# Optimization experiments

Measured on AMD Instinct MI355X. Metric: run time of the kernel, lower is better.

The kernel has to match this reference:

```python
import jax, jax.numpy as jnp
import numpy as np
import math

NEG = -10000.0  # original uses -10000.0, not -inf

def setup_inputs() -> dict:
    key = jax.random.key(0)
    B, S, H, D = 2, 2048, 16, 128
    qkv = jax.random.normal(key, (B, S, 3, H, D), dtype=jnp.float32)
    return {"qkv": qkv}

def reference(qkv):
    # qkv: (B, S, 3, H, D); causal softmax attention, dropout p=0 (identity)
    B, S, _, H, D = qkv.shape
    q = qkv[:, :, 0]  # (B,S,H,D)
    k = qkv[:, :, 1]
    v = qkv[:, :, 2]
    softmax_scale = 1.0 / math.sqrt(D)
    # scores: (B, H, T, S)
    scores = jnp.einsum('bthd,bshd->bhts', q, k * softmax_scale)
    causal_mask = jnp.triu(jnp.full((S, S), NEG, dtype=scores.dtype), 1)
    scores = scores + causal_mask  # broadcast over (B,H)
    attention = jax.nn.softmax(scores, axis=-1)
    out = jnp.einsum('bhts,bshd->bthd', attention, v)  # (B,T,H,D)
    return out
```

## Files before the change

kernel.cpp:

```cpp
#include <hip/hip_runtime.h>
#include <hip/hip_bf16.h>
#include <math.h>

typedef __bf16 bf16;
typedef bf16 bf16x8 __attribute__((ext_vector_type(8)));
typedef float floatx4 __attribute__((ext_vector_type(4)));

#define MFMA16(a, b, c) __builtin_amdgcn_mfma_f32_16x16x32_bf16(a, b, c, 0, 0, 0)

constexpr int Bb = 2, Ss = 2048, Hh = 16, Dd = 128;
constexpr float SCALE = 0.08838834764831845f;

__constant__ int U_QT[40] = {0,1,2,3, 4,4, 5,5, 6,6, 7,7, 8,8,8, 9,9,9, 10,10,10,
                             11,11,11, 12,12,12,12, 13,13,13,13, 14,14,14,14, 15,15,15,15};
__constant__ int U_S[40]  = {0,0,0,0, 0,10, 0,12, 0,14, 0,16, 0,12,24, 0,14,27, 0,15,30,
                             0,16,32, 0,13,26,39, 0,14,28,42, 0,15,30,45, 0,16,32,48};
__constant__ int U_E[40]  = {4,8,12,16, 10,20, 12,24, 14,28, 16,32, 12,24,36, 14,27,40,
                             15,30,44, 16,32,48, 13,26,39,52, 14,28,42,56, 15,30,45,60,
                             16,32,48,64};
__constant__ int RS0[12] = {0,2,4,6,8,11,14,17,20,24,28,32};
__constant__ int RN[12]  = {2,2,2,2,3,3,3,3,4,4,4,4};

__global__ __launch_bounds__(256) void prep_pack(const float* __restrict__ qkv,
                                                 bf16* __restrict__ QP,
                                                 bf16* __restrict__ KP,
                                                 bf16* __restrict__ VP) {
  __shared__ bf16 Vt[64 * 136];

  const int tid = threadIdx.x;
  const int w = tid >> 6, lane = tid & 63, quad = lane >> 4, l15 = lane & 15;
  const int qt = blockIdx.x, bh = blockIdx.y;
  const int b = bh >> 4, h = bh & 15;
  const int q0 = qt * 64;
  const size_t rs = (size_t)3 * Hh * Dd;
  const float* base = qkv + (size_t)b * Ss * rs + (size_t)h * Dd;

  for (int idx = tid; idx < 64 * 32; idx += 256) {
    const int row = idx >> 5;
    const int c4 = (idx & 31) << 2;
    const float* p = base + (size_t)(q0 + row) * rs + 2 * Hh * Dd + c4;
    float4 x = *(const float4*)p;
    bf16* d = Vt + row * 136 + c4;
    d[0] = (bf16)x.x; d[1] = (bf16)x.y; d[2] = (bf16)x.z; d[3] = (bf16)x.w;
  }

  {
    bf16* blob = QP + (size_t)(bh * 32 + qt) * 8192;
    const float* src = base + (size_t)(q0 + 4 * l15 + w) * rs;
    for (int kk = 0; kk < 4; ++kk) {
      const float* s8 = src + kk * 32 + quad * 8;
      float4 x0 = *(const float4*)s8, x1 = *(const float4*)(s8 + 4);
      bf16x8 f;
      f[0] = (bf16)(x0.x * SCALE); f[1] = (bf16)(x0.y * SCALE);
      f[2] = (bf16)(x0.z * SCALE); f[3] = (bf16)(x0.w * SCALE);
      f[4] = (bf16)(x1.x * SCALE); f[5] = (bf16)(x1.y * SCALE);
      f[6] = (bf16)(x1.z * SCALE); f[7] = (bf16)(x1.w * SCALE);
      *(bf16x8*)(blob + (size_t)(((w * 4 + kk) * 4 + quad) * 16 + l15) * 8) = f;
    }
  }

  const int ktg = qt * 2 + (w >> 1);
  {
    const int c = w & 1;
    bf16* blob = KP + (size_t)(bh * 64 + ktg) * 4096;
    const float* src = base + (size_t)(ktg * 32 + c * 16 + l15) * rs + Hh * Dd;
    for (int kk = 0; kk < 4; ++kk) {
      const float* s8 = src + kk * 32 + quad * 8;
      float4 x0 = *(const float4*)s8, x1 = *(const float4*)(s8 + 4);
      bf16x8 f;
      f[0] = (bf16)x0.x; f[1] = (bf16)x0.y; f[2] = (bf16)x0.z; f[3] = (bf16)x0.w;
      f[4] = (bf16)x1.x; f[5] = (bf16)x1.y; f[6] = (bf16)x1.z; f[7] = (bf16)x1.w;
      *(bf16x8*)(blob + (size_t)(((c * 4 + kk) * 4 + quad) * 16 + l15) * 8) = f;
    }
  }

  __syncthreads();

  {
    bf16* blob = VP + (size_t)(bh * 64 + ktg) * 4096;
    const int kloc = (w >> 1) * 32;
    for (int ti = 0; ti < 4; ++ti) {
      const int t = (w & 1) * 4 + ti;
      const int d = t * 16 + l15;
      bf16x8 f;
      for (int j = 0; j < 8; ++j) f[j] = Vt[(kloc + quad * 8 + j) * 136 + d];
      *(bf16x8*)(blob + (size_t)((t * 4 + quad) * 16 + l15) * 8) = f;
    }
  }
}

__device__ __forceinline__ void cp1k(const bf16* src, bf16* dst, int lane) {
  __builtin_amdgcn_global_load_lds(
      (__attribute__((address_space(1))) void*)(src + lane * 8),
      (__attribute__((address_space(3))) void*)dst, 16, 0, 0);
}

__global__ __launch_bounds__(256, 3) void attn_fwd_s(const bf16* __restrict__ QP,
                                                     const bf16* __restrict__ KP,
                                                     const bf16* __restrict__ VP,
                                                     float* __restrict__ out,
                                                     bf16* __restrict__ PO,
                                                     float* __restrict__ PL) {
  __shared__ bf16 Kl[2][4096];
  __shared__ bf16 Vl[2][4096];
  __shared__ bf16 Pl[4 * 32 * 40];

  const int tid = threadIdx.x;
  const int w = tid >> 6, lane = tid & 63, quad = lane >> 4, l15 = lane & 15;
  const int u = blockIdx.x;
  const int bh = blockIdx.y;
  const int b = bh >> 4, h = bh & 15;
  const int qt = U_QT[u];
  const int ks = U_S[u], ke = U_E[u];
  const int q0 = qt * 128;

  bf16x8 qf[2][4];
  for (int m = 0; m < 2; ++m) {
    const bf16* qp = QP + (size_t)(bh * 32 + 2 * qt + m) * 8192;
    for (int kk = 0; kk < 4; ++kk)
      qf[m][kk] = *(const bf16x8*)(qp + (size_t)(((w * 4 + kk) * 4 + quad) * 16 + l15) * 8);
  }

  floatx4 acc_o[2][8];
  for (int m = 0; m < 2; ++m)
    for (int t = 0; t < 8; ++t) acc_o[m][t] = (floatx4){0.f, 0.f, 0.f, 0.f};
  float l_part[2][4] = {{0.f, 0.f, 0.f, 0.f}, {0.f, 0.f, 0.f, 0.f}};

  const size_t bh64 = (size_t)bh * 64;
  bf16* pw = &Pl[w * 1280];

  auto stage = [&](int kt, int nb) {
    const bf16* kblob = KP + (bh64 + kt) * 4096;
    const bf16* vblob = VP + (bh64 + kt) * 4096;
    if (w < 2) {
      for (int i = 0; i < 4; ++i) {
        const int g = w * 4 + i;
        cp1k(kblob + g * 512, &Kl[nb][g * 512], lane);
      }
    } else {
      for (int i = 0; i < 4; ++i) {
        const int g = (w - 2) * 4 + i;
        cp1k(vblob + g * 512, &Vl[nb][g * 512], lane);
      }
    }
  };

  stage(ks, 0);
  __syncthreads();

  for (int it = 0, kt = ks; kt < ke; ++kt, ++it) {
    const int nb = it & 1;
    if (kt + 1 < ke) stage(kt + 1, nb ^ 1);

    const bool do0 = (kt <= 4 * qt + 1);
    const bool mask0 = (kt >= 4 * qt);
    const bool mask1 = (kt >= 4 * qt + 2);
    const int kbase = kt * 32;

    floatx4 s0[2], s1[2];
    s0[0] = s0[1] = s1[0] = s1[1] = (floatx4){0.f, 0.f, 0.f, 0.f};
    for (int c = 0; c < 2; ++c)
      for (int kk = 0; kk < 4; ++kk) {
        bf16x8 bfrag = *(const bf16x8*)(&Kl[nb][((c * 4 + kk) * 64 + lane) * 8]);
        if (do0) s0[c] = MFMA16(qf[0][kk], bfrag, s0[c]);
        s1[c] = MFMA16(qf[1][kk], bfrag, s1[c]);
      }

    if (do0) {
      float p[2][4];
      if (mask0) {
        for (int c = 0; c < 2; ++c) {
          const int colg = kbase + c * 16 + l15;
          for (int r = 0; r < 4; ++r) {
            const int rowg = q0 + 4 * (quad * 4 + r) + w;
            p[c][r] = __expf((colg > rowg) ? -10000.f : s0[c][r]);
          }
        }
      } else {
        for (int c = 0; c < 2; ++c)
          for (int r = 0; r < 4; ++r) p[c][r] = __expf(s0[c][r]);
      }
      for (int r = 0; r < 4; ++r) l_part[0][r] += p[0][r] + p[1][r];
      for (int c = 0; c < 2; ++c)
        for (int r = 0; r < 4; ++r)
          pw[(quad * 4 + r) * 40 + c * 16 + l15] = (bf16)p[c][r];
    }
    {
      float p[2][4];
      if (mask1) {
        for (int c = 0; c < 2; ++c) {
          const int colg = kbase + c * 16 + l15;
          for (int r = 0; r < 4; ++r) {
            const int rowg = q0 + 64 + 4 * (quad * 4 + r) + w;
            p[c][r] = __expf((colg > rowg) ? -10000.f : s1[c][r]);
          }
        }
      } else {
        for (int c = 0; c < 2; ++c)
          for (int r = 0; r < 4; ++r) p[c][r] = __expf(s1[c][r]);
      }
      for (int r = 0; r < 4; ++r) l_part[1][r] += p[0][r] + p[1][r];
      for (int c = 0; c < 2; ++c)
        for (int r = 0; r < 4; ++r)
          pw[(16 + quad * 4 + r) * 40 + c * 16 + l15] = (bf16)p[c][r];
    }

    bf16x8 af0, af1;
    if (do0) af0 = *(const bf16x8*)(&Pl[w * 1280 + l15 * 40 + quad * 8]);
    af1 = *(const bf16x8*)(&Pl[w * 1280 + (16 + l15) * 40 + quad * 8]);
    for (int t = 0; t < 8; ++t) {
      bf16x8 vfrag = *(const bf16x8*)(&Vl[nb][(t * 64 + lane) * 8]);
      if (do0) acc_o[0][t] = MFMA16(af0, vfrag, acc_o[0][t]);
      acc_o[1][t] = MFMA16(af1, vfrag, acc_o[1][t]);
    }

    __syncthreads();
  }

  if (u < 4) {
    for (int m = 0; m < 2; ++m) {
      float rl[4];
      for (int r = 0; r < 4; ++r) {
        float l = l_part[m][r];
        for (int off = 1; off < 16; off <<= 1) l += __shfl_xor(l, off);
        rl[r] = 1.0f / l;
      }
      for (int r = 0; r < 4; ++r) {
        const int rowg = q0 + m * 64 + 4 * (quad * 4 + r) + w;
        float* op = out + ((size_t)(b * Ss + rowg) * Hh + h) * Dd + l15;
        for (int t = 0; t < 8; ++t) op[t * 16] = acc_o[m][t][r] * rl[r];
      }
    }
  } else {
    const int slot = bh * 36 + (u - 4);
    bf16* po = PO + (size_t)slot * 16384;
    float* pl = PL + (size_t)slot * 128;
    for (int m = 0; m < 2; ++m) {
      for (int r = 0; r < 4; ++r) {
        float l = l_part[m][r];
        for (int off = 1; off < 16; off <<= 1) l += __shfl_xor(l, off);
        if (l15 == 0) pl[m * 64 + 4 * (quad * 4 + r) + w] = l;
      }
      for (int r = 0; r < 4; ++r) {
        const int rloc = m * 64 + 4 * (quad * 4 + r) + w;
        bf16* pp = po + rloc * 128 + l15;
        for (int t = 0; t < 8; ++t) pp[t * 16] = (bf16)acc_o[m][t][r];
      }
    }
  }
}

__global__ __launch_bounds__(256) void reduce_merge(const bf16* __restrict__ PO,
                                                    const float* __restrict__ PL,
                                                    float* __restrict__ out) {
  const int qt = 4 + blockIdx.x;
  const int bh = blockIdx.y;
  const int b = bh >> 4, h = bh & 15;
  const int s0 = bh * 36 + RS0[blockIdx.x];
  const int nch = RN[blockIdx.x];
  const int tid = threadIdx.x;

  __shared__ float linv[128];
  if (tid < 128) {
    float l = 0.f;
    for (int c = 0; c < nch; ++c) l += PL[(size_t)(s0 + c) * 128 + tid];
    linv[tid] = 1.0f / l;
  }
  __syncthreads();

  const int q0 = qt * 128;
  for (int t = 0; t < 32; ++t) {
    const int idx2 = t * 256 + tid;
    const int row = idx2 >> 6;
    const int d = (idx2 & 63) * 2;
    float v0 = 0.f, v1 = 0.f;
    for (int c = 0; c < nch; ++c) {
      const bf16* p = PO + (size_t)(s0 + c) * 16384 + row * 128 + d;
      v0 += (float)p[0];
      v1 += (float)p[1];
    }
    float* op = out + ((size_t)(b * Ss + q0 + row) * Hh + h) * Dd + d;
    const float rl = linv[row];
    op[0] = v0 * rl;
    op[1] = v1 * rl;
  }
}

__global__ __launch_bounds__(256, 3) void attn_fwd_mono(const bf16* __restrict__ QP,
                                                        const bf16* __restrict__ KP,
                                                        const bf16* __restrict__ VP,
                                                        float* __restrict__ out) {
  __shared__ bf16 Kl[2][4096];
  __shared__ bf16 Vl[2][4096];
  __shared__ bf16 Pl[4 * 32 * 40];

  const int tid = threadIdx.x;
  const int w = tid >> 6, lane = tid & 63, quad = lane >> 4, l15 = lane & 15;
  const int qt = (gridDim.x - 1) - blockIdx.x;
  const int bh = blockIdx.y;
  const int b = bh >> 4, h = bh & 15;
  const int q0 = qt * 128;

  bf16x8 qf[2][4];
  for (int m = 0; m < 2; ++m) {
    const bf16* qp = QP + (size_t)(bh * 32 + 2 * qt + m) * 8192;
    for (int kk = 0; kk < 4; ++kk)
      qf[m][kk] = *(const bf16x8*)(qp + (size_t)(((w * 4 + kk) * 4 + quad) * 16 + l15) * 8);
  }

  floatx4 acc_o[2][8];
  for (int m = 0; m < 2; ++m)
    for (int t = 0; t < 8; ++t) acc_o[m][t] = (floatx4){0.f, 0.f, 0.f, 0.f};
  float l_part[2][4] = {{0.f, 0.f, 0.f, 0.f}, {0.f, 0.f, 0.f, 0.f}};

  const int ntiles = 4 * qt + 4;
  const size_t bh64 = (size_t)bh * 64;
  bf16* pw = &Pl[w * 1280];

  auto stage = [&](int kt, int nb) {
    const bf16* kblob = KP + (bh64 + kt) * 4096;
    const bf16* vblob = VP + (bh64 + kt) * 4096;
    if (w < 2) {
      for (int i = 0; i < 4; ++i) {
        const int g = w * 4 + i;
        cp1k(kblob + g * 512, &Kl[nb][g * 512], lane);
      }
    } else {
      for (int i = 0; i < 4; ++i) {
        const int g = (w - 2) * 4 + i;
        cp1k(vblob + g * 512, &Vl[nb][g * 512], lane);
      }
    }
  };

  stage(0, 0);
  __syncthreads();

  for (int kt = 0; kt < ntiles; ++kt) {
    const int nb = kt & 1;
    if (kt + 1 < ntiles) stage(kt + 1, nb ^ 1);

    const bool do0 = (kt <= 4 * qt + 1);
    const bool mask0 = (kt >= 4 * qt);
    const bool mask1 = (kt >= 4 * qt + 2);
    const int kbase = kt * 32;

    floatx4 s0[2], s1[2];
    s0[0] = s0[1] = s1[0] = s1[1] = (floatx4){0.f, 0.f, 0.f, 0.f};
    for (int c = 0; c < 2; ++c)
      for (int kk = 0; kk < 4; ++kk) {
        bf16x8 bfrag = *(const bf16x8*)(&Kl[nb][((c * 4 + kk) * 64 + lane) * 8]);
        if (do0) s0[c] = MFMA16(qf[0][kk], bfrag, s0[c]);
        s1[c] = MFMA16(qf[1][kk], bfrag, s1[c]);
      }

    if (do0) {
      float p[2][4];
      if (mask0) {
        for (int c = 0; c < 2; ++c) {
          const int colg = kbase + c * 16 + l15;
          for (int r = 0; r < 4; ++r) {
            const int rowg = q0 + 4 * (quad * 4 + r) + w;
            p[c][r] = __expf((colg > rowg) ? -10000.f : s0[c][r]);
          }
        }
      } else {
        for (int c = 0; c < 2; ++c)
          for (int r = 0; r < 4; ++r) p[c][r] = __expf(s0[c][r]);
      }
      for (int r = 0; r < 4; ++r) l_part[0][r] += p[0][r] + p[1][r];
      for (int c = 0; c < 2; ++c)
        for (int r = 0; r < 4; ++r)
          pw[(quad * 4 + r) * 40 + c * 16 + l15] = (bf16)p[c][r];
    }
    {
      float p[2][4];
      if (mask1) {
        for (int c = 0; c < 2; ++c) {
          const int colg = kbase + c * 16 + l15;
          for (int r = 0; r < 4; ++r) {
            const int rowg = q0 + 64 + 4 * (quad * 4 + r) + w;
            p[c][r] = __expf((colg > rowg) ? -10000.f : s1[c][r]);
          }
        }
      } else {
        for (int c = 0; c < 2; ++c)
          for (int r = 0; r < 4; ++r) p[c][r] = __expf(s1[c][r]);
      }
      for (int r = 0; r < 4; ++r) l_part[1][r] += p[0][r] + p[1][r];
      for (int c = 0; c < 2; ++c)
        for (int r = 0; r < 4; ++r)
          pw[(16 + quad * 4 + r) * 40 + c * 16 + l15] = (bf16)p[c][r];
    }

    bf16x8 af0, af1;
    if (do0) af0 = *(const bf16x8*)(&Pl[w * 1280 + l15 * 40 + quad * 8]);
    af1 = *(const bf16x8*)(&Pl[w * 1280 + (16 + l15) * 40 + quad * 8]);
    for (int t = 0; t < 8; ++t) {
      bf16x8 vfrag = *(const bf16x8*)(&Vl[nb][(t * 64 + lane) * 8]);
      if (do0) acc_o[0][t] = MFMA16(af0, vfrag, acc_o[0][t]);
      acc_o[1][t] = MFMA16(af1, vfrag, acc_o[1][t]);
    }

    __syncthreads();
  }

  for (int m = 0; m < 2; ++m) {
    float rl[4];
    for (int r = 0; r < 4; ++r) {
      float l = l_part[m][r];
      for (int off = 1; off < 16; off <<= 1) l += __shfl_xor(l, off);
      rl[r] = 1.0f / l;
    }
    for (int r = 0; r < 4; ++r) {
      const int rowg = q0 + m * 64 + 4 * (quad * 4 + r) + w;
      float* op = out + ((size_t)(b * Ss + rowg) * Hh + h) * Dd + l15;
      for (int t = 0; t < 8; ++t) op[t * 16] = acc_o[m][t][r] * rl[r];
    }
  }
}

extern "C" void kernel_launch(void* const* d_in, const int* in_sizes, int n_in,
                              void* d_out, int out_size, void* d_ws, size_t ws_size,
                              hipStream_t stream) {
  const float* qkv = (const float*)d_in[0];
  float* out = (float*)d_out;
  char* ws = (char*)d_ws;
  bf16* QP = (bf16*)ws;
  bf16* KP = (bf16*)(ws + (size_t)16 * 1024 * 1024);
  bf16* VP = (bf16*)(ws + (size_t)32 * 1024 * 1024);
  bf16* PO = (bf16*)(ws + (size_t)48 * 1024 * 1024);
  float* PL = (float*)(ws + (size_t)48 * 1024 * 1024 + (size_t)1152 * 32768);

  const size_t need = (size_t)48 * 1024 * 1024 + (size_t)1152 * 32768 + (size_t)1152 * 512;

  prep_pack<<<dim3(32, 32), 256, 0, stream>>>(qkv, QP, KP, VP);
  if (ws_size >= need) {
    attn_fwd_s<<<dim3(40, 32), 256, 0, stream>>>(QP, KP, VP, out, PO, PL);
    reduce_merge<<<dim3(12, 32), 256, 0, stream>>>(PO, PL, out);
  } else {
    attn_fwd_mono<<<dim3(16, 32), 256, 0, stream>>>(QP, KP, VP, out);
  }
}
```

Before: 259.8 us.

## Flatten grids bh-fastest, stage partial stores through LDS, vectorize merge kernel

Grids move from 2D to 1D with the batch-head index varying fastest. This changes block dispatch order so that blocks sharing a query tile run together, which should improve L2 locality and balance heavy causal tiles across CUs. The split-K partial outputs are now staged through shared memory and written with 16-byte coalesced stores instead of scattered 2-byte stores. The merge kernel now uses 512 threads, each reading 16-byte bf16 vectors and writing float4 outputs. The cost is extra syncthreads in the epilogue and higher register use in the reduce kernel.

After: 231.0 us. 1.12x faster.

```diff
diff --git a/kernel.cpp b/kernel.cpp
--- a/kernel.cpp
+++ b/kernel.cpp
@@ -29,7 +29,7 @@
 
   const int tid = threadIdx.x;
   const int w = tid >> 6, lane = tid & 63, quad = lane >> 4, l15 = lane & 15;
-  const int qt = blockIdx.x, bh = blockIdx.y;
+  const int bh = blockIdx.x & 31, qt = blockIdx.x >> 5;
   const int b = bh >> 4, h = bh & 15;
   const int q0 = qt * 64;
   const size_t rs = (size_t)3 * Hh * Dd;
@@ -107,8 +107,8 @@
 
   const int tid = threadIdx.x;
   const int w = tid >> 6, lane = tid & 63, quad = lane >> 4, l15 = lane & 15;
-  const int u = blockIdx.x;
-  const int bh = blockIdx.y;
+  const int bh = blockIdx.x & 31;
+  const int u = blockIdx.x >> 5;
   const int b = bh >> 4, h = bh & 15;
   const int qt = U_QT[u];
   const int ks = U_S[u], ke = U_E[u];
@@ -235,54 +235,67 @@
     const int slot = bh * 36 + (u - 4);
     bf16* po = PO + (size_t)slot * 16384;
     float* pl = PL + (size_t)slot * 128;
+    bf16* Ol = &Kl[0][0];
     for (int m = 0; m < 2; ++m) {
       for (int r = 0; r < 4; ++r) {
         float l = l_part[m][r];
         for (int off = 1; off < 16; off <<= 1) l += __shfl_xor(l, off);
         if (l15 == 0) pl[m * 64 + 4 * (quad * 4 + r) + w] = l;
       }
+      __syncthreads();
       for (int r = 0; r < 4; ++r) {
-        const int rloc = m * 64 + 4 * (quad * 4 + r) + w;
-        bf16* pp = po + rloc * 128 + l15;
-        for (int t = 0; t < 8; ++t) pp[t * 16] = (bf16)acc_o[m][t][r];
-      }
-    }
-  }
-}
-
-__global__ __launch_bounds__(256) void reduce_merge(const bf16* __restrict__ PO,
+        const int rl = 4 * (quad * 4 + r) + w;
+        bf16* op = Ol + rl * 128 + l15;
+        for (int t = 0; t < 8; ++t) op[t * 16] = (bf16)acc_o[m][t][r];
+      }
+      __syncthreads();
+      for (int k = 0; k < 4; ++k) {
+        bf16x8 v = *(const bf16x8*)(Ol + k * 2048 + tid * 8);
+        *(bf16x8*)(po + m * 8192 + k * 2048 + tid * 8) = v;
+      }
+    }
+  }
+}
+
+__global__ __launch_bounds__(512) void reduce_merge(const bf16* __restrict__ PO,
                                                     const float* __restrict__ PL,
                                                     float* __restrict__ out) {
-  const int qt = 4 + blockIdx.x;
-  const int bh = blockIdx.y;
+  const int bh = blockIdx.x & 31;
+  const int j = blockIdx.x >> 5;
   const int b = bh >> 4, h = bh & 15;
-  const int s0 = bh * 36 + RS0[blockIdx.x];
-  const int nch = RN[blockIdx.x];
+  const int s0 = bh * 36 + RS0[j];
+  const int nch = RN[j];
   const int tid = threadIdx.x;
-
-  __shared__ float linv[128];
-  if (tid < 128) {
-    float l = 0.f;
-    for (int c = 0; c < nch; ++c) l += PL[(size_t)(s0 + c) * 128 + tid];
-    linv[tid] = 1.0f / l;
-  }
-  __syncthreads();
-
-  const int q0 = qt * 128;
-  for (int t = 0; t < 32; ++t) {
-    const int idx2 = t * 256 + tid;
-    const int row = idx2 >> 6;
-    const int d = (idx2 & 63) * 2;
-    float v0 = 0.f, v1 = 0.f;
-    for (int c = 0; c < nch; ++c) {
-      const bf16* p = PO + (size_t)(s0 + c) * 16384 + row * 128 + d;
-      v0 += (float)p[0];
-      v1 += (float)p[1];
-    }
-    float* op = out + ((size_t)(b * Ss + q0 + row) * Hh + h) * Dd + d;
-    const float rl = linv[row];
-    op[0] = v0 * rl;
-    op[1] = v1 * rl;
+  const int row = tid >> 2;
+  const int d0 = (tid & 3) << 5;
+
+  float l = 0.f;
+  for (int c = 0; c < nch; ++c) l += PL[(size_t)(s0 + c) * 128 + row];
+  const float rl = 1.0f / l;
+
+  float acc[32];
+#pragma unroll
+  for (int e = 0; e < 32; ++e) acc[e] = 0.f;
+  for (int c = 0; c < nch; ++c) {
+    const bf16* p = PO + (size_t)(s0 + c) * 16384 + row * 128 + d0;
+#pragma unroll
+    for (int k = 0; k < 4; ++k) {
+      bf16x8 v = *(const bf16x8*)(p + k * 8);
+#pragma unroll
+      for (int e = 0; e < 8; ++e) acc[k * 8 + e] += (float)v[e];
+    }
+  }
+
+  const int q0 = (4 + j) * 128;
+  float* op = out + ((size_t)(b * Ss + q0 + row) * Hh + h) * Dd + d0;
+#pragma unroll
+  for (int k = 0; k < 8; ++k) {
+    float4 o;
+    o.x = acc[k * 4 + 0] * rl;
+    o.y = acc[k * 4 + 1] * rl;
+    o.z = acc[k * 4 + 2] * rl;
+    o.w = acc[k * 4 + 3] * rl;
+    *(float4*)(op + k * 4) = o;
   }
 }
 
@@ -434,10 +447,10 @@
 
   const size_t need = (size_t)48 * 1024 * 1024 + (size_t)1152 * 32768 + (size_t)1152 * 512;
 
-  prep_pack<<<dim3(32, 32), 256, 0, stream>>>(qkv, QP, KP, VP);
+  prep_pack<<<dim3(1024), 256, 0, stream>>>(qkv, QP, KP, VP);
   if (ws_size >= need) {
-    attn_fwd_s<<<dim3(40, 32), 256, 0, stream>>>(QP, KP, VP, out, PO, PL);
-    reduce_merge<<<dim3(12, 32), 256, 0, stream>>>(PO, PL, out);
+    attn_fwd_s<<<dim3(1280), 256, 0, stream>>>(QP, KP, VP, out, PO, PL);
+    reduce_merge<<<dim3(384), 512, 0, stream>>>(PO, PL, out);
   } else {
     attn_fwd_mono<<<dim3(16, 32), 256, 0, stream>>>(QP, KP, VP, out);
   }
```
